# Performance work log

Measured on AMD Instinct MI355X. Metric: run time of the kernel, lower is better.

## Reference

```python
import jax, jax.numpy as jnp
import numpy as np

TAU = 0.2  # world.kgc_temp
EPS = 1e-12  # F.normalize eps


def _l2_normalize(z):
    n = jnp.linalg.norm(z, axis=1, keepdims=True)
    return z / jnp.maximum(n, EPS)


def setup_inputs() -> dict:
    key = jax.random.key(0)
    k1, k2 = jax.random.split(key)
    N, D = 8192, 512
    z1 = jax.random.normal(k1, (N, D), dtype=jnp.float32)
    z2 = jax.random.normal(k2, (N, D), dtype=jnp.float32)
    return {"z1": z1, "z2": z2}


def _semi_loss(h1, h2):
    # h1, h2: [N, D] already L2-normalized
    refl_sim = jnp.exp(jnp.matmul(h1, h1.T) / TAU)      # [N, N]
    between_sim = jnp.exp(jnp.matmul(h1, h2.T) / TAU)   # [N, N]
    denom = refl_sim.sum(axis=1) + between_sim.sum(axis=1) - jnp.diag(refl_sim)
    return -jnp.log(jnp.diag(between_sim) / denom)      # [N]


def reference(z1, z2):
    h1 = _l2_normalize(z1)
    h2 = _l2_normalize(z2)
    l1 = _semi_loss(h1, h2)
    l2 = _semi_loss(h2, h1)
    return jnp.sum((l1 + l2) * 0.5)
```

## Files before the change

kernel.cpp:

```cpp
#include <hip/hip_runtime.h>
#include <hip/hip_bf16.h>
#include <math.h>
#include <stdint.h>

#define N_ROWS 8192
#define DIM 512
#define INV_TAU 5.0f
#define EXP5 148.41315910257660342f

typedef float f32x4 __attribute__((ext_vector_type(4)));
typedef long long i64;

union PairU {
  int4 v;
  struct { i64 lo, hi; } s;
};

__device__ __forceinline__ void gload_lds16(const void* g, void* l) {
  __builtin_amdgcn_global_load_lds(
      (__attribute__((address_space(1))) void*)(void*)g,
      (__attribute__((address_space(3))) void*)l,
      16, 0, 0);
}

__global__ __launch_bounds__(256) void normalize_kernel(
    const float* __restrict__ z1, const float* __restrict__ z2,
    uint8_t* __restrict__ h1p, uint8_t* __restrict__ h2p,
    float* __restrict__ dvec,
    float* __restrict__ r1, float* __restrict__ r2,
    float* __restrict__ brow, float* __restrict__ bcol,
    float* __restrict__ out) {
  __shared__ __align__(16) uint8_t L[16384];
  const int t = threadIdx.x;
  const int lr = t >> 4;
  const int kb = t & 15;
  const int row = blockIdx.x * 16 + lr;
  const float4* p1 = (const float4*)(z1 + (size_t)row * DIM + kb * 32);
  const float4* p2 = (const float4*)(z2 + (size_t)row * DIM + kb * 32);
  float4 a[8], b[8];
  float s1 = 0.f, s2 = 0.f, s3 = 0.f;
#pragma unroll
  for (int i = 0; i < 8; i++) {
    a[i] = p1[i]; b[i] = p2[i];
    s1 += a[i].x*a[i].x + a[i].y*a[i].y + a[i].z*a[i].z + a[i].w*a[i].w;
    s2 += b[i].x*b[i].x + b[i].y*b[i].y + b[i].z*b[i].z + b[i].w*b[i].w;
    s3 += a[i].x*b[i].x + a[i].y*b[i].y + a[i].z*b[i].z + a[i].w*b[i].w;
  }
  for (int m = 1; m <= 8; m <<= 1) {
    s1 += __shfl_xor(s1, m);
    s2 += __shfl_xor(s2, m);
    s3 += __shfl_xor(s3, m);
  }
  const float inv1 = 1.0f / fmaxf(sqrtf(s1), 1e-12f);
  const float inv2 = 1.0f / fmaxf(sqrtf(s2), 1e-12f);
  int w1[8], w2[8];
#pragma unroll
  for (int i = 0; i < 8; i++) {
    int w = __builtin_amdgcn_cvt_pk_fp8_f32(a[i].x*inv1, a[i].y*inv1, 0, false);
    w1[i] = __builtin_amdgcn_cvt_pk_fp8_f32(a[i].z*inv1, a[i].w*inv1, w, true);
    w = __builtin_amdgcn_cvt_pk_fp8_f32(b[i].x*inv2, b[i].y*inv2, 0, false);
    w2[i] = __builtin_amdgcn_cvt_pk_fp8_f32(b[i].z*inv2, b[i].w*inv2, w, true);
  }
  union { i64 q; int d[2]; } u;
  const int lbase = (kb >> 1) * 1024 + lr * 16 + (kb & 1) * 8;
#pragma unroll
  for (int q = 0; q < 4; q++) {
    u.d[0] = w1[q*2]; u.d[1] = w1[q*2+1];
    *(i64*)(L + lbase + q * 256) = u.q;
    u.d[0] = w2[q*2]; u.d[1] = w2[q*2+1];
    *(i64*)(L + 8192 + lbase + q * 256) = u.q;
  }
  if (kb == 0) dvec[row] = s3 * inv1 * inv2;
  if (t < 16) {
    const int i = blockIdx.x * 16 + t;
    r1[i] = 0.f; r2[i] = 0.f; brow[i] = 0.f; bcol[i] = 0.f;
    if (i == 0) out[0] = 0.f;
  }
  __syncthreads();
  const size_t gb = (size_t)blockIdx.x * 8192;
  int4* g1 = (int4*)(h1p + gb);
  int4* g2 = (int4*)(h2p + gb);
  const int4* Lv = (const int4*)L;
  g1[t]       = Lv[t];
  g1[t + 256] = Lv[t + 256];
  g2[t]       = Lv[t + 512];
  g2[t + 256] = Lv[t + 768];
}

__global__ __launch_bounds__(256, 2) void expsum_kernel(
    const uint8_t* __restrict__ h1p, const uint8_t* __restrict__ h2p,
    float* __restrict__ r1, float* __restrict__ r2,
    float* __restrict__ brow, float* __restrict__ bcol) {
  __shared__ __align__(16) uint8_t Bs[65536];

  const int u = (blockIdx.x & 7) * 1032 + (blockIdx.x >> 3);
  int bj = (int)((sqrt(8.0 * (double)u + 1.0) - 1.0) * 0.5);
  if (bj * (bj + 1) / 2 > u) bj--;
  if ((bj + 1) * (bj + 2) / 2 <= u) bj++;
  const int bi = u - bj * (bj + 1) / 2;
  const bool diagb = (bi == bj);

  const uint8_t* Ap = (bi < 64) ? h1p : h2p;
  const uint8_t* Bp = (bj < 64) ? h1p : h2p;
  float* rowsOut = (bi < 64) ? ((bj < 64) ? r1 : brow) : r2;
  float* colsOut = (bj < 64) ? r1 : ((bi < 64) ? bcol : r2);
  const int iOutBase = (bi & 63) * 128;
  const int jOutBase = (bj & 63) * 128;

  const int t = threadIdx.x;
  const int w = t >> 6;
  const int lane = t & 63;
  const int l16 = lane & 15;
  const int kq = lane >> 4;

  const uint8_t* Abase =
      Ap + ((size_t)((bi & 63) * 8 + w * 2)) * 8192 + (size_t)lane * 16 + 3584;
  const uint8_t* aSt0 = Abase;
  const uint8_t* aSt1 = Abase + 8192;

  PairU Ar[3][2];
#pragma unroll
  for (int p = 0; p < 2; p++) {
    const int ofs = p * 1024 - 3584;
    Ar[p][0].v = *(const int4*)(aSt0 + ofs);
    Ar[p][1].v = *(const int4*)(aSt1 + ofs);
  }

  {
    const uint8_t* Bgp = Bp + (size_t)(bj & 63) * 65536;
#pragma unroll
    for (int rnd = 0; rnd < 16; rnd++)
      gload_lds16(Bgp + rnd * 4096 + t * 16, Bs + rnd * 4096 + t * 16);
  }

  f32x4 acc[2][8];
#pragma unroll
  for (int a = 0; a < 2; a++)
#pragma unroll
    for (int b = 0; b < 8; b++)
#pragma unroll
      for (int r = 0; r < 4; r++) acc[a][b][r] = 0.0f;

  __syncthreads();

#pragma unroll
  for (int kbp = 0; kbp < 8; kbp++) {
    const int cur = kbp % 3;
    if (kbp < 6) {
      const int nxt = (kbp + 2) % 3;
      const int ofs = (kbp + 2) * 1024 - 3584;
      Ar[nxt][0].v = *(const int4*)(aSt0 + ofs);
      Ar[nxt][1].v = *(const int4*)(aSt1 + ofs);
    }
    PairU Bf[8];
#pragma unroll
    for (int f = 0; f < 8; f++)
      Bf[f].v = *(const int4*)(Bs + f * 8192 + kbp * 1024 + lane * 16);
#pragma unroll
    for (int fm = 0; fm < 2; fm++)
#pragma unroll
      for (int fn = 0; fn < 8; fn++)
        acc[fm][fn] = __builtin_amdgcn_mfma_f32_16x16x32_fp8_fp8(
            Ar[cur][fm].s.lo, Bf[fn].s.lo, acc[fm][fn], 0, 0, 0);
#pragma unroll
    for (int fm = 0; fm < 2; fm++)
#pragma unroll
      for (int fn = 0; fn < 8; fn++)
        acc[fm][fn] = __builtin_amdgcn_mfma_f32_16x16x32_fp8_fp8(
            Ar[cur][fm].s.hi, Bf[fn].s.hi, acc[fm][fn], 0, 0, 0);
  }

  float rowp[2][4];
  float colp[8];
#pragma unroll
  for (int fm = 0; fm < 2; fm++)
#pragma unroll
    for (int r = 0; r < 4; r++) rowp[fm][r] = 0.0f;
#pragma unroll
  for (int fn = 0; fn < 8; fn++) colp[fn] = 0.0f;

  if (!diagb) {
#pragma unroll
    for (int fm = 0; fm < 2; fm++)
#pragma unroll
      for (int fn = 0; fn < 8; fn++)
#pragma unroll
        for (int r = 0; r < 4; r++) {
          const float e = __expf(acc[fm][fn][r] * INV_TAU);
          rowp[fm][r] += e;
          colp[fn] += e;
        }
  } else {
#pragma unroll
    for (int fm = 0; fm < 2; fm++)
#pragma unroll
      for (int fn = 0; fn < 8; fn++)
#pragma unroll
        for (int r = 0; r < 4; r++) {
          const int ti = w * 32 + fm * 16 + kq * 4 + r;
          const int tj = fn * 16 + l16;
          const float e = __expf(acc[fm][fn][r] * INV_TAU);
          rowp[fm][r] += (ti <= tj) ? e : 0.0f;
          colp[fn] += (ti < tj) ? e : 0.0f;
        }
  }

  __syncthreads();
  float* lds_row = (float*)Bs;
  float* lds_col = lds_row + 128;
  if (t < 128) lds_row[t] = 0.0f; else if (t < 256) lds_col[t - 128] = 0.0f;
  __syncthreads();

#pragma unroll
  for (int fm = 0; fm < 2; fm++) {
#pragma unroll
    for (int r = 0; r < 4; r++) {
      float v = rowp[fm][r];
      v += __shfl_xor(v, 1);
      v += __shfl_xor(v, 2);
      v += __shfl_xor(v, 4);
      v += __shfl_xor(v, 8);
      if (l16 == 0) atomicAdd(&lds_row[w * 32 + fm * 16 + kq * 4 + r], v);
    }
  }
#pragma unroll
  for (int fn = 0; fn < 8; fn++) {
    float v = colp[fn];
    v += __shfl_xor(v, 16);
    v += __shfl_xor(v, 32);
    if (kq == 0) atomicAdd(&lds_col[fn * 16 + l16], v);
  }
  __syncthreads();

  if (t < 128) atomicAdd(&rowsOut[iOutBase + t], lds_row[t]);
  else         atomicAdd(&colsOut[jOutBase + (t - 128)], lds_col[t - 128]);
}

__global__ __launch_bounds__(256) void finalize_kernel(
    const float* __restrict__ r1, const float* __restrict__ r2,
    const float* __restrict__ brow, const float* __restrict__ bcol,
    const float* __restrict__ dvec, float* __restrict__ out) {
  const int i = blockIdx.x * 256 + threadIdx.x;
  const float den1 = r1[i] + brow[i] - EXP5;
  const float den2 = r2[i] + bcol[i] - EXP5;
  float v = 0.5f * (logf(den1) + logf(den2)) - INV_TAU * dvec[i];
  for (int m = 32; m; m >>= 1) v += __shfl_xor(v, m);
  __shared__ float red[4];
  const int wave = threadIdx.x >> 6;
  if ((threadIdx.x & 63) == 0) red[wave] = v;
  __syncthreads();
  if (threadIdx.x == 0) atomicAdd(out, red[0] + red[1] + red[2] + red[3]);
}

extern "C" void kernel_launch(void* const* d_in, const int* in_sizes, int n_in,
                              void* d_out, int out_size, void* d_ws, size_t ws_size,
                              hipStream_t stream) {
  const float* z1 = (const float*)d_in[0];
  const float* z2 = (const float*)d_in[1];
  float* out = (float*)d_out;

  char* ws = (char*)d_ws;
  uint8_t* h1p = (uint8_t*)ws;
  uint8_t* h2p = (uint8_t*)(ws + (4u << 20));
  float* r1   = (float*)(ws + (8u << 20));
  float* r2   = r1 + N_ROWS;
  float* brow = r2 + N_ROWS;
  float* bcol = brow + N_ROWS;
  float* dvec = bcol + N_ROWS;

  normalize_kernel<<<N_ROWS / 16, 256, 0, stream>>>(
      z1, z2, h1p, h2p, dvec, r1, r2, brow, bcol, out);
  expsum_kernel<<<8256, 256, 0, stream>>>(h1p, h2p, r1, r2, brow, bcol);
  finalize_kernel<<<N_ROWS / 256, 256, 0, stream>>>(r1, r2, brow, bcol, dvec, out);
}
```

Baseline: 222.1 us.

## Enlarge expsum tiles to 256x128 with 512-thread blocks over triangular grid

Each block of the fused exp-sum kernel now covers 256 rows by 128 columns using eight waves instead of four, which halves the block count to 4160. The triangular tile enumeration is rewritten so that predication is needed only on the two tiles that straddle the diagonal. The 64KB B tile loaded into LDS is now shared by twice as many rows, which cuts B global traffic and per-block overhead. In exchange it adds masked work on the diagonal tiles and more wasted compute there, and requests launch bounds of 512 threads with 4 blocks per CU, which may not fit given 64KB LDS per block.

```diff
diff --git a/kernel.cpp b/kernel.cpp
--- a/kernel.cpp
+++ b/kernel.cpp
@@ -87,25 +87,27 @@
   g2[t + 256] = Lv[t + 768];
 }
 
-__global__ __launch_bounds__(256, 2) void expsum_kernel(
+__global__ __launch_bounds__(512, 4) void expsum_kernel(
     const uint8_t* __restrict__ h1p, const uint8_t* __restrict__ h2p,
     float* __restrict__ r1, float* __restrict__ r2,
     float* __restrict__ brow, float* __restrict__ bcol) {
   __shared__ __align__(16) uint8_t Bs[65536];
 
-  const int u = (blockIdx.x & 7) * 1032 + (blockIdx.x >> 3);
-  int bj = (int)((sqrt(8.0 * (double)u + 1.0) - 1.0) * 0.5);
-  if (bj * (bj + 1) / 2 > u) bj--;
-  if ((bj + 1) * (bj + 2) / 2 <= u) bj++;
-  const int bi = u - bj * (bj + 1) / 2;
-  const bool diagb = (bi == bj);
-
-  const uint8_t* Ap = (bi < 64) ? h1p : h2p;
+  const int u = (blockIdx.x & 7) * 520 + (blockIdx.x >> 3);
+  int bi = (int)((129.0 - sqrt(129.0 * 129.0 - 4.0 * (double)u)) * 0.5);
+  while (bi * (129 - bi) > u) bi--;
+  while ((bi + 1) * (128 - bi) <= u) bi++;
+  const int bj = 2 * bi + (u - bi * (129 - bi));
+  const bool needPred = (bj == 2 * bi) || (bj == 2 * bi + 1);
+
+  const uint8_t* Ap = (bi < 32) ? h1p : h2p;
   const uint8_t* Bp = (bj < 64) ? h1p : h2p;
-  float* rowsOut = (bi < 64) ? ((bj < 64) ? r1 : brow) : r2;
-  float* colsOut = (bj < 64) ? r1 : ((bi < 64) ? bcol : r2);
-  const int iOutBase = (bi & 63) * 128;
+  float* rowsOut = (bi < 32) ? ((bj < 64) ? r1 : brow) : r2;
+  float* colsOut = (bj < 64) ? r1 : ((bi < 32) ? bcol : r2);
+  const int iOutBase = (bi & 31) * 256;
   const int jOutBase = (bj & 63) * 128;
+  const int giBase = bi * 256;
+  const int gjBase = bj * 128;
 
   const int t = threadIdx.x;
   const int w = t >> 6;
@@ -114,7 +116,7 @@
   const int kq = lane >> 4;
 
   const uint8_t* Abase =
-      Ap + ((size_t)((bi & 63) * 8 + w * 2)) * 8192 + (size_t)lane * 16 + 3584;
+      Ap + ((size_t)((bi & 31) * 16 + w * 2)) * 8192 + (size_t)lane * 16 + 3584;
   const uint8_t* aSt0 = Abase;
   const uint8_t* aSt1 = Abase + 8192;
 
@@ -129,8 +131,8 @@
   {
     const uint8_t* Bgp = Bp + (size_t)(bj & 63) * 65536;
 #pragma unroll
-    for (int rnd = 0; rnd < 16; rnd++)
-      gload_lds16(Bgp + rnd * 4096 + t * 16, Bs + rnd * 4096 + t * 16);
+    for (int rnd = 0; rnd < 8; rnd++)
+      gload_lds16(Bgp + rnd * 8192 + t * 16, Bs + rnd * 8192 + t * 16);
   }
 
   f32x4 acc[2][8];
@@ -179,7 +181,7 @@
 #pragma unroll
   for (int fn = 0; fn < 8; fn++) colp[fn] = 0.0f;
 
-  if (!diagb) {
+  if (!needPred) {
 #pragma unroll
     for (int fm = 0; fm < 2; fm++)
 #pragma unroll
@@ -197,18 +199,18 @@
       for (int fn = 0; fn < 8; fn++)
 #pragma unroll
         for (int r = 0; r < 4; r++) {
-          const int ti = w * 32 + fm * 16 + kq * 4 + r;
-          const int tj = fn * 16 + l16;
+          const int gi = giBase + w * 32 + fm * 16 + kq * 4 + r;
+          const int gj = gjBase + fn * 16 + l16;
           const float e = __expf(acc[fm][fn][r] * INV_TAU);
-          rowp[fm][r] += (ti <= tj) ? e : 0.0f;
-          colp[fn] += (ti < tj) ? e : 0.0f;
+          rowp[fm][r] += (gi <= gj) ? e : 0.0f;
+          colp[fn] += (gi < gj) ? e : 0.0f;
         }
   }
 
   __syncthreads();
-  float* lds_row = (float*)Bs;
-  float* lds_col = lds_row + 128;
-  if (t < 128) lds_row[t] = 0.0f; else if (t < 256) lds_col[t - 128] = 0.0f;
+  float* lds_col = (float*)Bs;
+  float* lds_row = lds_col + 128;
+  if (t < 128) lds_col[t] = 0.0f;
   __syncthreads();
 
 #pragma unroll
@@ -220,7 +222,7 @@
       v += __shfl_xor(v, 2);
       v += __shfl_xor(v, 4);
       v += __shfl_xor(v, 8);
-      if (l16 == 0) atomicAdd(&lds_row[w * 32 + fm * 16 + kq * 4 + r], v);
+      if (l16 == 0) lds_row[w * 32 + fm * 16 + kq * 4 + r] = v;
     }
   }
 #pragma unroll
@@ -232,8 +234,8 @@
   }
   __syncthreads();
 
-  if (t < 128) atomicAdd(&rowsOut[iOutBase + t], lds_row[t]);
-  else         atomicAdd(&colsOut[jOutBase + (t - 128)], lds_col[t - 128]);
+  if (t < 256) atomicAdd(&rowsOut[iOutBase + t], lds_row[t]);
+  else if (t < 384) atomicAdd(&colsOut[jOutBase + (t - 256)], lds_col[t - 256]);
 }
 
 __global__ __launch_bounds__(256) void finalize_kernel(
@@ -270,6 +272,6 @@
 
   normalize_kernel<<<N_ROWS / 16, 256, 0, stream>>>(
       z1, z2, h1p, h2p, dvec, r1, r2, brow, bcol, out);
-  expsum_kernel<<<8256, 256, 0, stream>>>(h1p, h2p, r1, r2, brow, bcol);
+  expsum_kernel<<<4160, 512, 0, stream>>>(h1p, h2p, r1, r2, brow, bcol);
   finalize_kernel<<<N_ROWS / 256, 256, 0, stream>>>(r1, r2, brow, bcol, dvec, out);
 }
```

Result: faster. 207.4 us (-6.6%).

## Switch to MI355 scaled 16x16x128 FP8 MFMA with reorganized fragment layout

Applied to the files above, without the earlier changes.

Replaces the 16x16x32 FP8 MFMA with the gfx950 scaled 16x16x128 f8f6f4 instruction, using unit scales (0x7F exponent). The packed fp8 layout written by the normalize kernel and the A/B fragment loads in the expsum kernel are reorganized to match the 32-byte-per-lane operand format. All A fragments are now preloaded into registers instead of using a rotating triple buffer. The occupancy hint of 2 blocks per CU is dropped, and row partials are stored directly instead of via LDS atomics. The aim is to cut MFMA instruction count and raise matrix throughput, at the cost of higher register pressure and a new data layout that must match exactly.

```diff
diff --git a/kernel.cpp b/kernel.cpp
--- a/kernel.cpp
+++ b/kernel.cpp
@@ -9,11 +9,12 @@
 #define EXP5 148.41315910257660342f
 
 typedef float f32x4 __attribute__((ext_vector_type(4)));
-typedef long long i64;
-
-union PairU {
-  int4 v;
-  struct { i64 lo, hi; } s;
+typedef int   i32x4 __attribute__((ext_vector_type(4)));
+typedef int   i32x8 __attribute__((ext_vector_type(8)));
+
+union Frag8 {
+  i32x8 v8;
+  struct { i32x4 lo, hi; } s;
 };
 
 __device__ __forceinline__ void gload_lds16(const void* g, void* l) {
@@ -61,15 +62,12 @@
     w = __builtin_amdgcn_cvt_pk_fp8_f32(b[i].x*inv2, b[i].y*inv2, 0, false);
     w2[i] = __builtin_amdgcn_cvt_pk_fp8_f32(b[i].z*inv2, b[i].w*inv2, w, true);
   }
-  union { i64 q; int d[2]; } u;
-  const int lbase = (kb >> 1) * 1024 + lr * 16 + (kb & 1) * 8;
-#pragma unroll
-  for (int q = 0; q < 4; q++) {
-    u.d[0] = w1[q*2]; u.d[1] = w1[q*2+1];
-    *(i64*)(L + lbase + q * 256) = u.q;
-    u.d[0] = w2[q*2]; u.d[1] = w2[q*2+1];
-    *(i64*)(L + 8192 + lbase + q * 256) = u.q;
-  }
+  const int ks = kb >> 2;
+  const int l = (kb & 3) * 16 + lr;
+  *(int4*)(L + ks * 2048 + l * 16)          = make_int4(w1[0], w1[1], w1[2], w1[3]);
+  *(int4*)(L + ks * 2048 + 1024 + l * 16)   = make_int4(w1[4], w1[5], w1[6], w1[7]);
+  *(int4*)(L + 8192 + ks * 2048 + l * 16)        = make_int4(w2[0], w2[1], w2[2], w2[3]);
+  *(int4*)(L + 8192 + ks * 2048 + 1024 + l * 16) = make_int4(w2[4], w2[5], w2[6], w2[7]);
   if (kb == 0) dvec[row] = s3 * inv1 * inv2;
   if (t < 16) {
     const int i = blockIdx.x * 16 + t;
@@ -87,7 +85,7 @@
   g2[t + 256] = Lv[t + 768];
 }
 
-__global__ __launch_bounds__(256, 2) void expsum_kernel(
+__global__ __launch_bounds__(256) void expsum_kernel(
     const uint8_t* __restrict__ h1p, const uint8_t* __restrict__ h2p,
     float* __restrict__ r1, float* __restrict__ r2,
     float* __restrict__ brow, float* __restrict__ bcol) {
@@ -113,18 +111,17 @@
   const int l16 = lane & 15;
   const int kq = lane >> 4;
 
-  const uint8_t* Abase =
-      Ap + ((size_t)((bi & 63) * 8 + w * 2)) * 8192 + (size_t)lane * 16 + 3584;
-  const uint8_t* aSt0 = Abase;
-  const uint8_t* aSt1 = Abase + 8192;
-
-  PairU Ar[3][2];
-#pragma unroll
-  for (int p = 0; p < 2; p++) {
-    const int ofs = p * 1024 - 3584;
-    Ar[p][0].v = *(const int4*)(aSt0 + ofs);
-    Ar[p][1].v = *(const int4*)(aSt1 + ofs);
-  }
+  const uint8_t* Ag =
+      Ap + ((size_t)((bi & 63) * 8 + w * 2)) * 8192 + (size_t)lane * 16 + 4096;
+  Frag8 Af[2][4];
+#pragma unroll
+  for (int f = 0; f < 2; f++)
+#pragma unroll
+    for (int ks = 0; ks < 4; ks++) {
+      const int ofs = f * 8192 + ks * 2048 - 4096;
+      Af[f][ks].s.lo = *(const i32x4*)(Ag + ofs);
+      Af[f][ks].s.hi = *(const i32x4*)(Ag + ofs + 1024);
+    }
 
   {
     const uint8_t* Bgp = Bp + (size_t)(bj & 63) * 65536;
@@ -141,33 +138,27 @@
 #pragma unroll
       for (int r = 0; r < 4; r++) acc[a][b][r] = 0.0f;
 
-  __syncthreads();
-
-#pragma unroll
-  for (int kbp = 0; kbp < 8; kbp++) {
-    const int cur = kbp % 3;
-    if (kbp < 6) {
-      const int nxt = (kbp + 2) % 3;
-      const int ofs = (kbp + 2) * 1024 - 3584;
-      Ar[nxt][0].v = *(const int4*)(aSt0 + ofs);
-      Ar[nxt][1].v = *(const int4*)(aSt1 + ofs);
+  const uint8_t* BsL = Bs + lane * 16;
+
+  __syncthreads();
+
+#pragma unroll
+  for (int ks = 0; ks < 4; ks++) {
+    Frag8 Bf[8];
+#pragma unroll
+    for (int fn = 0; fn < 8; fn++) {
+      Bf[fn].s.lo = *(const i32x4*)(BsL + fn * 8192 + ks * 2048);
+      Bf[fn].s.hi = *(const i32x4*)(BsL + fn * 8192 + ks * 2048 + 1024);
     }
-    PairU Bf[8];
-#pragma unroll
-    for (int f = 0; f < 8; f++)
-      Bf[f].v = *(const int4*)(Bs + f * 8192 + kbp * 1024 + lane * 16);
 #pragma unroll
     for (int fm = 0; fm < 2; fm++)
 #pragma unroll
       for (int fn = 0; fn < 8; fn++)
-        acc[fm][fn] = __builtin_amdgcn_mfma_f32_16x16x32_fp8_fp8(
-            Ar[cur][fm].s.lo, Bf[fn].s.lo, acc[fm][fn], 0, 0, 0);
-#pragma unroll
-    for (int fm = 0; fm < 2; fm++)
-#pragma unroll
-      for (int fn = 0; fn < 8; fn++)
-        acc[fm][fn] = __builtin_amdgcn_mfma_f32_16x16x32_fp8_fp8(
-            Ar[cur][fm].s.hi, Bf[fn].s.hi, acc[fm][fn], 0, 0, 0);
+        acc[fm][fn] = __builtin_amdgcn_mfma_scale_f32_16x16x128_f8f6f4(
+            Af[fm][ks].v8, Bf[fn].v8, acc[fm][fn],
+            0, 0,
+            0, 0x7F7F7F7F,
+            0, 0x7F7F7F7F);
   }
 
   float rowp[2][4];
@@ -206,9 +197,9 @@
   }
 
   __syncthreads();
-  float* lds_row = (float*)Bs;
-  float* lds_col = lds_row + 128;
-  if (t < 128) lds_row[t] = 0.0f; else if (t < 256) lds_col[t - 128] = 0.0f;
+  float* lds_col = (float*)Bs;
+  float* lds_row = lds_col + 128;
+  if (t < 128) lds_col[t] = 0.0f;
   __syncthreads();
 
 #pragma unroll
@@ -220,7 +211,7 @@
       v += __shfl_xor(v, 2);
       v += __shfl_xor(v, 4);
       v += __shfl_xor(v, 8);
-      if (l16 == 0) atomicAdd(&lds_row[w * 32 + fm * 16 + kq * 4 + r], v);
+      if (l16 == 0) lds_row[w * 32 + fm * 16 + kq * 4 + r] = v;
     }
   }
 #pragma unroll
```

After: 200.1 us. 9.9% less time.
